# Optimization experiments

Hardware: AMD Instinct MI355X
Metric: run time of the kernel (lower is better)

## Reference

```python
import jax, jax.numpy as jnp
import numpy as np

N = 4096
DEG = 16.0
KC = 64  # max closed-neighborhood size supported (deg~16 graph => safe)


def setup_inputs() -> dict:
    key = jax.random.key(0)
    ks = jax.random.split(key, 6)
    u = jax.random.uniform(ks[0], (N, N))
    upper = jnp.triu((u < (DEG / N)).astype(jnp.float32), k=1)
    adj = upper + upper.T  # symmetric 0/1, zero diagonal
    d = 64
    return {
        'adj': adj,
        'e_w': jax.random.normal(ks[1], (15, d), dtype=jnp.float32) * 0.25,
        'e_b': jnp.zeros((d,), jnp.float32),
        'w1': jax.random.normal(ks[2], (3, d, d), dtype=jnp.float32) * 0.125,
        'b1': jnp.zeros((3, d), jnp.float32),
        'w2': jax.random.normal(ks[3], (3, d, d), dtype=jnp.float32) * 0.125,
        'b2': jnp.zeros((3, d), jnp.float32),
        'eps': jnp.zeros((3,), jnp.float32),
    }


def cr_feat(adj):
    n = adj.shape[0]
    m = adj + jnp.eye(n, dtype=adj.dtype)  # closed-neighborhood indicator rows [N,N]
    k = m.sum(1)                            # |S_v|
    D = m @ adj                             # D[v,u] = degree of u inside S_v (A symmetric)
    E = 0.5 * jnp.sum(m * D, axis=1)        # edges inside S_v
    W = jnp.sum(m * D * (D - 1.0) * 0.5, axis=1)  # wedges inside S_v
    vals, idx = jax.lax.top_k(m, KC)        # members of S_v (padded)
    valid = (vals > 0.5).astype(adj.dtype)
    sub = adj[idx[:, :, None], idx[:, None, :]]        # [N,KC,KC] induced subgraph
    sub = sub * valid[:, :, None] * valid[:, None, :]
    T = jnp.einsum('vij,vjk,vki->v', sub, sub, sub) / 6.0  # triangles inside S_v
    f3 = T
    f2 = W - 3.0 * T
    f1 = E * (k - 2.0) - 2.0 * f2 - 3.0 * f3
    tot = k * (k - 1.0) * (k - 2.0) / 6.0   # C(k,3) = total triples
    f0 = tot - f1 - f2 - f3
    f = jnp.stack([f0, f1, f2, f3], axis=1)
    f = jnp.where((k >= 3.0)[:, None], f, 0.0)  # original skips |nb|<3
    return f / (jnp.sum(f, axis=1, keepdims=True) + 1e-10)


def ww_feat(adj):
    a2 = adj @ adj
    a4 = a2 @ a2                             # matrix_power(adj, 4)
    vals, _ = jax.lax.top_k(a4, 8)           # per-row sort desc, top 8
    return vals


def degree_feat(adj):
    d = adj.sum(1)
    diag_a2 = jnp.einsum('vu,uv->v', adj, adj)  # diag(A@A)
    return jnp.stack([d, d ** 2, diag_a2], axis=1)


def _forward(adj, e_w, e_b, w1, b1, w2, b2, eps):
    feats = jnp.concatenate([cr_feat(adj), ww_feat(adj), degree_feat(adj)], axis=1)  # [N,15]
    x = feats @ e_w + e_b
    for i in range(3):
        h = (1.0 + eps[i]) * x + adj @ x
        x = jax.nn.relu(h @ w1[i] + b1[i]) @ w2[i] + b2[i]
    return x.sum(0)


def reference(adj, e_w, e_b, w1, b1, w2, b2, eps):
    return _forward(adj, e_w, e_b, w1, b1, w2, b2, eps)
```

## Files before the change

kernel.cpp:

```cpp
#include <hip/hip_runtime.h>
#include <hip/hip_bf16.h>
#include <stdint.h>

#define NN 4096


__device__ __forceinline__ unsigned int wave_umax_bcast(unsigned int v) {
    int x = (int)v;
    x = max(x, __builtin_amdgcn_update_dpp(0, x, 0x111, 0xF, 0xF, true));
    x = max(x, __builtin_amdgcn_update_dpp(0, x, 0x112, 0xF, 0xF, true));
    x = max(x, __builtin_amdgcn_update_dpp(0, x, 0x114, 0xF, 0xF, true));
    x = max(x, __builtin_amdgcn_update_dpp(0, x, 0x118, 0xF, 0xF, true));
    x = max(x, __builtin_amdgcn_update_dpp(0, x, 0x142, 0xF, 0xF, true));
    x = max(x, __builtin_amdgcn_update_dpp(0, x, 0x143, 0xF, 0xF, true));
    return (unsigned int)__builtin_amdgcn_readlane(x, 63);
}

__global__ __launch_bounds__(256) void scan_k(const float* __restrict__ adj,
                                              int* __restrict__ nbr,
                                              int* __restrict__ deg,
                                              unsigned long long* __restrict__ abits,
                                              float* __restrict__ feats) {
    __shared__ int nlist[4][64];
    int tid = threadIdx.x;
    int wv = tid >> 6, ln = tid & 63;
    int v = blockIdx.x * 4 + wv;
    size_t rb = (size_t)v * NN;
    int total = 0;
    unsigned long long w0 = 0;
    const float4* row4 = (const float4*)(adj + rb);
    for (int base = 0; base < NN; base += 256) {
        float4 f = row4[(base >> 2) + ln];
        int q4 = (base >> 8) << 2;
        #pragma unroll
        for (int j = 0; j < 4; j++) {
            float vj = (j == 0) ? f.x : (j == 1) ? f.y : (j == 2) ? f.z : f.w;
            unsigned long long m = __ballot(vj > 0.5f);
            if (vj > 0.5f) {
                int pos = total + __popcll(m & ((1ull << ln) - 1ull));
                if (pos < 64) nlist[wv][pos] = base + 4 * ln + j;
            }
            if (ln == q4 + j) w0 = m;
            total += __popcll(m);
        }
    }
    abits[(size_t)v * 64 + ln] = w0;
    int degL = min(total, 64);
    if (ln < degL) nbr[v * 64 + ln] = nlist[wv][ln];
    if (ln == 0) {
        deg[v] = total;
        float degf = (float)total;
        feats[v * 16 + 12] = degf;
        feats[v * 16 + 13] = degf * degf;
        feats[v * 16 + 14] = degf;
    }
}

__global__ __launch_bounds__(256) void cra2_k(const unsigned long long* __restrict__ abits,
                                              const int* __restrict__ nbr,
                                              const int* __restrict__ deg,
                                              unsigned int* __restrict__ a3n,
                                              unsigned int* __restrict__ side,
                                              unsigned int* __restrict__ scnt,
                                              float* __restrict__ feats) {
    __shared__ __align__(64) unsigned int smem[NN + 196 + 640];
    int tid = threadIdx.x;
    int bid = blockIdx.x;
    int wv = tid >> 6, ln = tid & 63;

    if (bid < NN) {
        unsigned int* acc   = smem;
        int* us             = (int*)(smem + NN);
        int* dus            = (int*)(smem + NN + 64);
        unsigned int* pbase = smem + NN + 128;
        unsigned int* wsumS = smem + NN + 192;
        unsigned int* plist = smem + NN + 196;
        int v = bid;
        uint4 z = {0u, 0u, 0u, 0u};
        #pragma unroll
        for (int i = 0; i < 4; i++) ((uint4*)acc)[tid + 256 * i] = z;
        int dv = min(deg[v], 64);
        if (tid < 64) {
            int u = (tid < dv) ? nbr[v * 64 + tid] : 0;
            us[tid] = u;
            int du = (tid < dv) ? min(deg[u], 64) : 0;
            dus[tid] = du;
            int incl = du;
            #pragma unroll
            for (int off = 1; off < 64; off <<= 1) {
                int n = __shfl_up(incl, off, 64);
                if (tid >= off) incl += n;
            }
            pbase[tid] = (unsigned int)(incl - du);
            if (tid == 63) wsumS[0] = (unsigned int)incl;
        }
        __syncthreads();
        int npair = (int)min(wsumS[0], 640u);
        for (int p = tid; p < dv * 64; p += 256) {
            int i = p >> 6, j = p & 63;
            if (j < dus[i]) {
                unsigned int pos = pbase[i] + (unsigned int)j;
                if (pos < 640u) {
                    unsigned int w = (unsigned int)nbr[us[i] * 64 + j];
                    plist[pos] = w | ((unsigned int)min(deg[w], 64) << 12);
                }
            }
        }
        __syncthreads();
        int lim64 = ((npair + 1) >> 1) << 6;
        for (int q = tid; q < lim64; q += 256) {
            int s = ((q >> 6) << 1) | ((q >> 5) & 1);
            int j = q & 31;
            if (s < npair) {
                unsigned int e = plist[s];
                int dgw = (int)(e >> 12);
                const int* nrw = nbr + (e & 0xFFFu) * 64;
                if (j < dgw) atomicAdd(&acc[nrw[j]], 1u);
                if (j == 31) {
                    for (int jj = 32; jj < dgw; jj++) atomicAdd(&acc[nrw[jj]], 1u);
                }
            }
        }
        __syncthreads();
        unsigned int wA = 0, wB = 0, ovm = 0;
        #pragma unroll
        for (int k = 0; k < 8; k++) {
            unsigned int a = acc[tid + 512 * k];
            wA |= min(a, 15u) << (4 * k);
            ovm |= (a > 15u ? 1u : 0u) << k;
        }
        #pragma unroll
        for (int k = 0; k < 8; k++) {
            unsigned int a = acc[tid + 256 + 512 * k];
            wB |= min(a, 15u) << (4 * k);
            ovm |= (a > 15u ? 1u : 0u) << (8 + k);
        }
        a3n[(size_t)v * 512 + tid] = wA;
        a3n[(size_t)v * 512 + tid + 256] = wB;
        int lov = __popc(ovm);
        int inc2 = lov;
        #pragma unroll
        for (int off = 1; off < 64; off <<= 1) {
            int n = __shfl_up(inc2, off, 64);
            if (ln >= off) inc2 += n;
        }
        if (ln == 63) wsumS[wv] = (unsigned int)inc2;
        __syncthreads();
        unsigned int wpre2 = 0, totS = 0;
        #pragma unroll
        for (int q = 0; q < 4; q++) {
            unsigned int s = wsumS[q];
            if (q < wv) wpre2 += s;
            totS += s;
        }
        unsigned int pos2 = wpre2 + (unsigned int)(inc2 - lov);
        unsigned int* sideR = side + (size_t)v * 192;
        while (ovm) {
            int i2 = __ffs(ovm) - 1;
            ovm &= ovm - 1;
            unsigned int col = (i2 < 8) ? (unsigned int)(tid + 512 * i2)
                                        : (unsigned int)(tid + 256 + 512 * (i2 - 8));
            unsigned int a = acc[col];
            if (pos2 < 192u) sideR[pos2] = ((a - 15u) << 16) | col;
            pos2++;
        }
        if (tid == 0) scnt[v] = min(totS, 192u);
    } else {
        unsigned long long* rows = (unsigned long long*)smem;
        int* mems = (int*)(smem + 1024);
        int v = (bid - NN) * 4 + wv;

        int dv = deg[v];
        int degL = min(dv, 64);
        int c = min(dv + 1, 64);

        int nl = (ln < degL) ? nbr[v * 64 + ln] : 0;
        int isless = (ln < degL && nl < v) ? 1 : 0;
        int pos = isless;
        #pragma unroll
        for (int off = 32; off; off >>= 1) pos += __shfl_xor(pos, off, 64);

        int mem = 0;
        if (ln < c) {
            if (ln < pos)       mem = nl;
            else if (ln == pos) mem = v;
            else                mem = nbr[v * 64 + ln - 1];
        }
        mems[wv * 64 + ln] = mem;
        __syncthreads();

        unsigned long long mask = 0ull;
        {
            const unsigned long long* rowb = abits + (size_t)mem * 64;
            for (int j = 0; j < c; j++) {
                int mj = mems[wv * 64 + j];
                unsigned long long w = rowb[((mj >> 8) << 2) | (mj & 3)];
                mask |= ((w >> ((mj >> 2) & 63)) & 1ull) << j;
            }
        }
        if (ln >= c) mask = 0ull;
        rows[wv * 64 + ln] = mask;
        __syncthreads();

        int tpart = 0;
        float epart = 0.f, wpart = 0.f;
        if (ln < c) {
            unsigned long long mm = mask;
            while (mm) {
                int j = __ffsll(mm) - 1;
                mm &= mm - 1;
                tpart += __popcll(mask & rows[wv * 64 + j]);
            }
            if (ln != pos) {
                int cn = __popcll(rows[wv * 64 + pos] & mask);
                float D2 = (float)cn + 1.0f;
                epart = D2;
                wpart = D2 * (D2 - 1.0f) * 0.5f;
            }
        }
        float es = epart, wsum2 = wpart;
        int ts = tpart;
        #pragma unroll
        for (int off = 32; off; off >>= 1) {
            es += __shfl_xor(es, off, 64);
            wsum2 += __shfl_xor(wsum2, off, 64);
            ts += __shfl_xor(ts, off, 64);
        }

        if (ln == 0) {
            float degf = (float)dv;
            float k = degf + 1.0f;
            float E = 0.5f * (es + degf);
            float W = wsum2 + degf * (degf - 1.0f) * 0.5f;
            float T = (float)ts / 6.0f;
            float f3 = T;
            float f2 = W - 3.0f * T;
            float f1 = E * (k - 2.0f) - 2.0f * f2 - 3.0f * f3;
            float tot2 = k * (k - 1.0f) * (k - 2.0f) / 6.0f;
            float f0 = tot2 - f1 - f2 - f3;
            if (k < 3.0f) { f0 = f1 = f2 = f3 = 0.f; }
            float s = f0 + f1 + f2 + f3 + 1e-10f;
            feats[v * 16 + 0] = f0 / s;
            feats[v * 16 + 1] = f1 / s;
            feats[v * 16 + 2] = f2 / s;
            feats[v * 16 + 3] = f3 / s;
        }
    }
}

__global__ __launch_bounds__(256) void a4row_k(const unsigned int* __restrict__ a3n,
                                               const unsigned int* __restrict__ side,
                                               const unsigned int* __restrict__ scnt,
                                               const int* __restrict__ deg,
                                               const int* __restrict__ nbr,
                                               const float* __restrict__ feats,
                                               const float* __restrict__ e_w,
                                               const float* __restrict__ e_b,
                                               float* __restrict__ x0) {
    __shared__ unsigned int sacc[NN];
    __shared__ unsigned int sbase[64];
    __shared__ unsigned int sbs[64];
    __shared__ unsigned int sS[64];
    __shared__ unsigned int wtops[32];
    int tid = threadIdx.x;
    int wv = tid >> 6, ln = tid & 63;
    int v = blockIdx.x;

    {
        uint4 z = {0u, 0u, 0u, 0u};
        #pragma unroll
        for (int i = 0; i < 4; i++) ((uint4*)sacc)[tid + 256 * i] = z;
    }
    int dvv = min(deg[v], 64);
    if (tid < dvv) {
        unsigned int u = (unsigned int)nbr[v * 64 + tid];
        sbase[tid] = u * 512u;
        sbs[tid]   = u * 192u;
        sS[tid]    = scnt[u];
    }
    __syncthreads();

    for (int i = wv; i < dvv; i += 4) {
        int ns = (int)sS[i];
        const unsigned int* sp = side + sbs[i];
        for (int g2 = ln; g2 < ns; g2 += 64) {
            unsigned int e = sp[g2];
            atomicAdd(&sacc[e & 0xFFFu], e >> 16);
        }
    }

    unsigned int aE0 = 0, aO0 = 0, aE1 = 0, aO1 = 0;
    unsigned int SE00 = 0, SE01 = 0, SO00 = 0, SO01 = 0;
    unsigned int SE10 = 0, SE11 = 0, SO10 = 0, SO11 = 0;
    for (int s0 = 0; s0 < dvv; s0 += 16) {
        int se = min(s0 + 16, dvv);
        for (int s = s0; s < se; s++) {
            uint2 W = ((const uint2*)(a3n + sbase[s]))[tid];
            aE0 += W.x & 0x0F0F0F0Fu;
            aO0 += (W.x >> 4) & 0x0F0F0F0Fu;
            aE1 += W.y & 0x0F0F0F0Fu;
            aO1 += (W.y >> 4) & 0x0F0F0F0Fu;
        }
        SE00 += __builtin_amdgcn_perm(0u, aE0, 0x0c010c00u);
        SE01 += __builtin_amdgcn_perm(0u, aE0, 0x0c030c02u);
        SO00 += __builtin_amdgcn_perm(0u, aO0, 0x0c010c00u);
        SO01 += __builtin_amdgcn_perm(0u, aO0, 0x0c030c02u);
        SE10 += __builtin_amdgcn_perm(0u, aE1, 0x0c010c00u);
        SE11 += __builtin_amdgcn_perm(0u, aE1, 0x0c030c02u);
        SO10 += __builtin_amdgcn_perm(0u, aO1, 0x0c010c00u);
        SO11 += __builtin_amdgcn_perm(0u, aO1, 0x0c030c02u);
        aE0 = 0; aO0 = 0; aE1 = 0; aO1 = 0;
    }
    __syncthreads();

    unsigned int vv[16];
    {
        uint2 u0 = ((uint2*)sacc)[tid];
        uint2 u1 = ((uint2*)sacc)[tid + 256];
        uint2 u2 = ((uint2*)sacc)[tid + 512];
        uint2 u3 = ((uint2*)sacc)[tid + 768];
        uint2 u4 = ((uint2*)sacc)[tid + 1024];
        uint2 u5 = ((uint2*)sacc)[tid + 1280];
        uint2 u6 = ((uint2*)sacc)[tid + 1536];
        uint2 u7 = ((uint2*)sacc)[tid + 1792];
        vv[0]  = (SE00 & 0xFFFFu) + u0.x;  vv[8]  = (SE10 & 0xFFFFu) + u0.y;
        vv[1]  = (SO00 & 0xFFFFu) + u1.x;  vv[9]  = (SO10 & 0xFFFFu) + u1.y;
        vv[2]  = (SE00 >> 16)     + u2.x;  vv[10] = (SE10 >> 16)     + u2.y;
        vv[3]  = (SO00 >> 16)     + u3.x;  vv[11] = (SO10 >> 16)     + u3.y;
        vv[4]  = (SE01 & 0xFFFFu) + u4.x;  vv[12] = (SE11 & 0xFFFFu) + u4.y;
        vv[5]  = (SO01 & 0xFFFFu) + u5.x;  vv[13] = (SO11 & 0xFFFFu) + u5.y;
        vv[6]  = (SE01 >> 16)     + u6.x;  vv[14] = (SE11 >> 16)     + u6.y;
        vv[7]  = (SO01 >> 16)     + u7.x;  vv[15] = (SO11 >> 16)     + u7.y;
    }

    unsigned int best[8];
    #pragma unroll
    for (int q = 0; q < 8; q++) best[q] = 0u;
    #pragma unroll
    for (int m = 0; m < 16; m++) {
        unsigned int val = vv[m];
        if (val > best[7]) {
            best[7] = val;
            #pragma unroll
            for (int s = 7; s > 0; s--) {
                if (best[s] > best[s - 1]) {
                    unsigned int t2 = best[s - 1]; best[s - 1] = best[s]; best[s] = t2;
                } else break;
            }
        }
    }

    unsigned int wave_val = 0u;
    #pragma unroll
    for (int r = 0; r < 8; r++) {
        unsigned int kmax = wave_umax_bcast((best[0] << 6) | (unsigned int)ln);
        if (ln == (int)(kmax & 63u)) {
            #pragma unroll
            for (int s = 0; s < 7; s++) best[s] = best[s + 1];
            best[7] = 0u;
        }
        if (ln == r) wave_val = kmax >> 6;
    }
    if (ln < 8) wtops[wv * 8 + ln] = wave_val;
    __syncthreads();

    if (wv == 0) {
        unsigned int cand = (ln < 32) ? wtops[ln] : 0u;
        unsigned int myv = 0u;
        #pragma unroll
        for (int r = 0; r < 8; r++) {
            unsigned int kmax = wave_umax_bcast((cand << 6) | (unsigned int)ln);
            if (ln == (int)(kmax & 63u)) cand = 0u;
            if (ln == r) myv = kmax >> 6;
        }
        int d = ln;
        float s = e_b[d];
        s += feats[v * 16 + 0]  * e_w[0 * 64 + d];
        s += feats[v * 16 + 1]  * e_w[1 * 64 + d];
        s += feats[v * 16 + 2]  * e_w[2 * 64 + d];
        s += feats[v * 16 + 3]  * e_w[3 * 64 + d];
        #pragma unroll
        for (int j = 0; j < 8; j++) {
            float mj = (float)(unsigned int)__shfl((int)myv, j, 64);
            s += mj * e_w[(4 + j) * 64 + d];
        }
        s += feats[v * 16 + 12] * e_w[12 * 64 + d];
        s += feats[v * 16 + 13] * e_w[13 * 64 + d];
        s += feats[v * 16 + 14] * e_w[14 * 64 + d];
        x0[(size_t)v * 64 + d] = s;
    }
}

__global__ __launch_bounds__(256) void layer_k(const float* __restrict__ xin,
                                               float* __restrict__ xout,
                                               const float* __restrict__ w1,
                                               const float* __restrict__ b1,
                                               const float* __restrict__ w2,
                                               const float* __restrict__ b2,
                                               const float* __restrict__ eps,
                                               const int* __restrict__ nbr,
                                               const int* __restrict__ deg,
                                               float* __restrict__ out,
                                               int li) {
    __shared__ float wL[4096];
    __shared__ float h[4][64], t[4][64];
    int tid = threadIdx.x;
    int wv = tid >> 6, d = tid & 63;
    int v = blockIdx.x * 4 + wv;

    {
        const float4* src = (const float4*)(w1 + li * 4096);
        #pragma unroll
        for (int i = 0; i < 4; i++) ((float4*)wL)[tid + 256 * i] = src[tid + 256 * i];
    }

    float xv = xin[(size_t)v * 64 + d];
    int dv = min(deg[v], 64);
    const int* nl = nbr + v * 64;
    float agg = 0.f;
    int j = 0;
    for (; j + 4 <= dv; j += 4) {
        int n0 = nl[j], n1 = nl[j + 1], n2 = nl[j + 2], n3 = nl[j + 3];
        float a0 = xin[(size_t)n0 * 64 + d];
        float a1 = xin[(size_t)n1 * 64 + d];
        float a2v = xin[(size_t)n2 * 64 + d];
        float a3 = xin[(size_t)n3 * 64 + d];
        agg += (a0 + a1) + (a2v + a3);
    }
    for (; j < dv; j++) agg += xin[(size_t)nl[j] * 64 + d];
    float hv = (1.0f + eps[li]) * xv + agg;
    h[wv][d] = hv;
    __syncthreads();

    float s = b1[li * 64 + d];
    #pragma unroll 8
    for (int k = 0; k < 64; k++) s += h[wv][k] * wL[k * 64 + d];
    s = fmaxf(s, 0.f);
    t[wv][d] = s;
    __syncthreads();

    {
        const float4* src = (const float4*)(w2 + li * 4096);
        #pragma unroll
        for (int i = 0; i < 4; i++) ((float4*)wL)[tid + 256 * i] = src[tid + 256 * i];
    }
    __syncthreads();

    float o = b2[li * 64 + d];
    #pragma unroll 8
    for (int k = 0; k < 64; k++) o += t[wv][k] * wL[k * 64 + d];
    if (li == 2) {
        h[wv][d] = o;
        __syncthreads();
        if (wv == 0)
            atomicAdd(&out[d], (h[0][d] + h[1][d]) + (h[2][d] + h[3][d]));
    } else {
        xout[(size_t)v * 64 + d] = o;
    }
}

extern "C" void kernel_launch(void* const* d_in, const int* in_sizes, int n_in,
                              void* d_out, int out_size, void* d_ws, size_t ws_size,
                              hipStream_t stream) {
    const float* adj = (const float*)d_in[0];
    const float* e_w = (const float*)d_in[1];
    const float* e_b = (const float*)d_in[2];
    const float* w1  = (const float*)d_in[3];
    const float* b1  = (const float*)d_in[4];
    const float* w2  = (const float*)d_in[5];
    const float* b2  = (const float*)d_in[6];
    const float* eps = (const float*)d_in[7];
    float* out = (float*)d_out;

    char* ws = (char*)d_ws;
    unsigned int*       a3n     = (unsigned int*)(ws);
    unsigned int*       side    = (unsigned int*)(ws + 8388608);
    unsigned int*       scnt    = (unsigned int*)(ws + 11534336);
    int*                nbr     = (int*)(ws + 25165824);
    int*                deg     = (int*)(ws + 26214400);
    float*              feats   = (float*)(ws + 26247168);
    float*              x0      = (float*)(ws + 26509312);
    float*              x1      = (float*)(ws + 27557888);
    unsigned long long* abits   = (unsigned long long*)(ws + 28868608);

    hipMemsetAsync(out, 0, 64 * sizeof(float), stream);
    scan_k<<<1024, 256, 0, stream>>>(adj, nbr, deg, abits, feats);
    cra2_k<<<5120, 256, 0, stream>>>(abits, nbr, deg, a3n, side, scnt, feats);
    a4row_k<<<4096, 256, 0, stream>>>(a3n, side, scnt, deg, nbr, feats, e_w, e_b, x0);
    layer_k<<<1024, 256, 0, stream>>>(x0, x1, w1, b1, w2, b2, eps, nbr, deg, out, 0);
    layer_k<<<1024, 256, 0, stream>>>(x1, x0, w1, b1, w2, b2, eps, nbr, deg, out, 1);
    layer_k<<<1024, 256, 0, stream>>>(x0, x1, w1, b1, w2, b2, eps, nbr, deg, out, 2);
}
```

Measured before the change: 241.4 us.

## Fold output zeroing into scan kernel, unroll atomic scatter, branchless top-8

After: 226.6 us. 1.07x faster.

```diff
diff --git a/kernel.cpp b/kernel.cpp
--- a/kernel.cpp
+++ b/kernel.cpp
@@ -20,11 +20,13 @@
                                               int* __restrict__ nbr,
                                               int* __restrict__ deg,
                                               unsigned long long* __restrict__ abits,
-                                              float* __restrict__ feats) {
+                                              float* __restrict__ feats,
+                                              float* __restrict__ out) {
     __shared__ int nlist[4][64];
     int tid = threadIdx.x;
     int wv = tid >> 6, ln = tid & 63;
     int v = blockIdx.x * 4 + wv;
+    if (blockIdx.x == 0 && tid < 64) out[tid] = 0.f;
     size_t rb = (size_t)v * NN;
     int total = 0;
     unsigned long long w0 = 0;
@@ -108,18 +110,34 @@
         }
         __syncthreads();
         int lim64 = ((npair + 1) >> 1) << 6;
-        for (int q = tid; q < lim64; q += 256) {
-            int s = ((q >> 6) << 1) | ((q >> 5) & 1);
-            int j = q & 31;
-            if (s < npair) {
-                unsigned int e = plist[s];
-                int dgw = (int)(e >> 12);
-                const int* nrw = nbr + (e & 0xFFFu) * 64;
-                if (j < dgw) atomicAdd(&acc[nrw[j]], 1u);
-                if (j == 31) {
-                    for (int jj = 32; jj < dgw; jj++) atomicAdd(&acc[nrw[jj]], 1u);
-                }
-            }
+        for (int q = tid; q < lim64; q += 1024) {
+            int qa = q, qb = q + 256, qc = q + 512, qd = q + 768;
+            int sa = ((qa >> 6) << 1) | ((qa >> 5) & 1), ja = qa & 31;
+            int sb = ((qb >> 6) << 1) | ((qb >> 5) & 1), jb = qb & 31;
+            int sc = ((qc >> 6) << 1) | ((qc >> 5) & 1), jc = qc & 31;
+            int sd = ((qd >> 6) << 1) | ((qd >> 5) & 1), jd = qd & 31;
+            unsigned int ea = (sa < npair) ? plist[sa] : 0u;
+            unsigned int eb = (qb < lim64 && sb < npair) ? plist[sb] : 0u;
+            unsigned int ec = (qc < lim64 && sc < npair) ? plist[sc] : 0u;
+            unsigned int ed = (qd < lim64 && sd < npair) ? plist[sd] : 0u;
+            int da = (int)(ea >> 12), db = (int)(eb >> 12);
+            int dc = (int)(ec >> 12), dd = (int)(ed >> 12);
+            const int* na = nbr + (ea & 0xFFFu) * 64;
+            const int* nb = nbr + (eb & 0xFFFu) * 64;
+            const int* nc = nbr + (ec & 0xFFFu) * 64;
+            const int* nd = nbr + (ed & 0xFFFu) * 64;
+            int xa = (ja < da) ? na[ja] : -1;
+            int xb = (jb < db) ? nb[jb] : -1;
+            int xc = (jc < dc) ? nc[jc] : -1;
+            int xd = (jd < dd) ? nd[jd] : -1;
+            if (xa >= 0) atomicAdd(&acc[xa], 1u);
+            if (xb >= 0) atomicAdd(&acc[xb], 1u);
+            if (xc >= 0) atomicAdd(&acc[xc], 1u);
+            if (xd >= 0) atomicAdd(&acc[xd], 1u);
+            if (ja == 31) { for (int jj = 32; jj < da; jj++) atomicAdd(&acc[na[jj]], 1u); }
+            if (jb == 31) { for (int jj = 32; jj < db; jj++) atomicAdd(&acc[nb[jj]], 1u); }
+            if (jc == 31) { for (int jj = 32; jj < dc; jj++) atomicAdd(&acc[nc[jj]], 1u); }
+            if (jd == 31) { for (int jj = 32; jj < dd; jj++) atomicAdd(&acc[nd[jj]], 1u); }
         }
         __syncthreads();
         unsigned int wA = 0, wB = 0, ovm = 0;
@@ -338,15 +356,12 @@
     for (int q = 0; q < 8; q++) best[q] = 0u;
     #pragma unroll
     for (int m = 0; m < 16; m++) {
-        unsigned int val = vv[m];
-        if (val > best[7]) {
-            best[7] = val;
-            #pragma unroll
-            for (int s = 7; s > 0; s--) {
-                if (best[s] > best[s - 1]) {
-                    unsigned int t2 = best[s - 1]; best[s - 1] = best[s]; best[s] = t2;
-                } else break;
-            }
+        unsigned int carry = vv[m];
+        #pragma unroll
+        for (int s = 0; s < 8; s++) {
+            unsigned int hi = max(best[s], carry);
+            carry = min(best[s], carry);
+            best[s] = hi;
         }
     }
 
@@ -483,8 +498,7 @@
     float*              x1      = (float*)(ws + 27557888);
     unsigned long long* abits   = (unsigned long long*)(ws + 28868608);
 
-    hipMemsetAsync(out, 0, 64 * sizeof(float), stream);
-    scan_k<<<1024, 256, 0, stream>>>(adj, nbr, deg, abits, feats);
+    scan_k<<<1024, 256, 0, stream>>>(adj, nbr, deg, abits, feats, out);
     cra2_k<<<5120, 256, 0, stream>>>(abits, nbr, deg, a3n, side, scnt, feats);
     a4row_k<<<4096, 256, 0, stream>>>(a3n, side, scnt, deg, nbr, feats, e_w, e_b, x0);
     layer_k<<<1024, 256, 0, stream>>>(x0, x1, w1, b1, w2, b2, eps, nbr, deg, out, 0);
```
